# Kernel tuning notes

Measured on AMD Instinct MI355X. Metric: run time of the kernel, lower is better.

Reference implementation:

```python
import jax, jax.numpy as jnp
import numpy as np

EPS = 1e-5

def layer_norm(x, alpha, beta):
    mean = jnp.mean(x, axis=-1, keepdims=True)
    var = jnp.mean(jnp.square(x - mean), axis=-1, keepdims=True)
    return alpha * ((x - mean) / jnp.sqrt(var + EPS)) + beta

def setup_inputs() -> dict:
    key = jax.random.key(0)
    B, S, D, H = 4, 2048, 1024, 16
    Dff = 4 * D
    ks = jax.random.split(key, 8)
    inp = {
        "x": jax.random.normal(ks[0], (B, S, D), jnp.float32),
        "attention_mask": jnp.ones((B, S), jnp.int32),
        "ln1_alpha": jnp.ones((D,), jnp.float32),
        "ln1_beta": jnp.zeros((D,), jnp.float32),
        "ln2_alpha": jnp.ones((D,), jnp.float32),
        "ln2_beta": jnp.zeros((D,), jnp.float32),
        "Wq": jax.random.normal(ks[1], (D, D), jnp.float32) * 0.05,
        "Wk": jax.random.normal(ks[2], (D, D), jnp.float32) * 0.05,
        "Wv": jax.random.normal(ks[3], (D, D), jnp.float32) * 0.05,
        "Wo": jax.random.normal(ks[4], (D, D), jnp.float32) * 0.05,
        "W1": jax.random.normal(ks[5], (D, Dff), jnp.float32) * 0.02,
        "b1": jnp.zeros((Dff,), jnp.float32),
        "W2": jax.random.normal(ks[6], (Dff, D), jnp.float32) * 0.02,
        "b2": jnp.zeros((D,), jnp.float32),
    }
    return inp

def reference(x, attention_mask, ln1_alpha, ln1_beta, ln2_alpha, ln2_beta,
              Wq, Wk, Wv, Wo, W1, b1, W2, b2):
    B, S, D = x.shape
    H = 16
    dh = D // H

    # LN1 + self-attention
    y = layer_norm(x, ln1_alpha, ln1_beta)
    Q = (y @ Wq).reshape(B, S, H, dh).transpose(0, 2, 1, 3)  # [B,H,S,dh]
    K = (y @ Wk).reshape(B, S, H, dh).transpose(0, 2, 1, 3)
    V = (y @ Wv).reshape(B, S, H, dh).transpose(0, 2, 1, 3)

    scores = jnp.einsum("bhqd,bhkd->bhqk", Q, K) / jnp.sqrt(jnp.float32(dh))
    causal = jnp.tril(jnp.ones((S, S), jnp.float32))  # [S,S]
    tmask = attention_mask.astype(jnp.float32)  # [B,S]
    amask = causal[None, None, :, :] * tmask[:, None, None, :] * tmask[:, None, :, None]
    scores = jnp.where(amask > 0, scores, jnp.float32(-1e30))
    attn = jax.nn.softmax(scores, axis=-1)
    # dropout omitted (deterministic inference)
    ctx = jnp.einsum("bhqk,bhkd->bhqd", attn, V)
    ctx = ctx.transpose(0, 2, 1, 3).reshape(B, S, D)
    x = x + ctx @ Wo

    # LN2 + GELU FFN
    y = layer_norm(x, ln2_alpha, ln2_beta)
    h = jax.nn.gelu(y @ W1 + b1, approximate=False)
    x = x + (h @ W2 + b2)
    return x
```

## Files before the change

### kernel.cpp

```cpp
#include <hip/hip_runtime.h>
#include <math.h>

typedef unsigned short u16;
typedef unsigned int u32;
typedef __attribute__((ext_vector_type(4))) unsigned short u16x4;
typedef __attribute__((ext_vector_type(8))) short bf16x8;
typedef __attribute__((ext_vector_type(4))) float f32x4;

#define B_ 4
#define S_ 2048
#define D_ 1024
#define H_ 16
#define NT (B_*S_)
#define DFF 4096

static __device__ __forceinline__ float bf2f(u16 u) {
    return __uint_as_float(((u32)u) << 16);
}
static __device__ __forceinline__ u16 f2bf(float f) {
    u32 u = __float_as_uint(f);
    u32 r = (u + 0x7fffu + ((u >> 16) & 1u)) >> 16;
    return (u16)r;
}
static __device__ __forceinline__ void gload_lds16(const void* g, void* l) {
    __builtin_amdgcn_global_load_lds(
        (const __attribute__((address_space(1))) void*)g,
        (__attribute__((address_space(3))) void*)l, 16, 0, 0);
}

__global__ void transpose_f2b4(const float* __restrict__ s0, const float* __restrict__ s1,
                               const float* __restrict__ s2, const float* __restrict__ s3,
                               u16* __restrict__ d0, u16* __restrict__ d1,
                               u16* __restrict__ d2, u16* __restrict__ d3,
                               int R, int C) {
    const float* in = s0; u16* out = d0;
    if (blockIdx.z == 1) { in = s1; out = d1; }
    else if (blockIdx.z == 2) { in = s2; out = d2; }
    else if (blockIdx.z == 3) { in = s3; out = d3; }
    __shared__ float t[32][33];
    int c0 = blockIdx.x * 32, r0 = blockIdx.y * 32;
    int x = threadIdx.x, y = threadIdx.y;
    #pragma unroll
    for (int i = 0; i < 4; i++)
        t[y + i*8][x] = in[(long)(r0 + y + i*8) * C + c0 + x];
    __syncthreads();
    #pragma unroll
    for (int i = 0; i < 4; i++)
        out[(long)(c0 + y + i*8) * R + r0 + x] = f2bf(t[x][y + i*8]);
}

__global__ void transpose_f2b(const float* __restrict__ in, u16* __restrict__ out,
                              int R, int C) {
    __shared__ float t[32][33];
    int c0 = blockIdx.x * 32, r0 = blockIdx.y * 32;
    int x = threadIdx.x, y = threadIdx.y;
    #pragma unroll
    for (int i = 0; i < 4; i++)
        t[y + i*8][x] = in[(long)(r0 + y + i*8) * C + c0 + x];
    __syncthreads();
    #pragma unroll
    for (int i = 0; i < 4; i++)
        out[(long)(c0 + y + i*8) * R + r0 + x] = f2bf(t[x][y + i*8]);
}

__global__ void transpose_v(const u16* __restrict__ V, u16* __restrict__ Vt) {
    __shared__ u16 t[32][33];
    int z = blockIdx.z; int b = z >> 4, h = z & 15;
    int s0 = blockIdx.x * 32, d0 = blockIdx.y * 32;
    int x = threadIdx.x, y = threadIdx.y;
    const u16* in = V + ((long)b * S_ + s0) * D_ + h * 64 + d0;
    #pragma unroll
    for (int i = 0; i < 4; i++)
        t[y + i*8][x] = in[(long)(y + i*8) * D_ + x];
    __syncthreads();
    u16* out = Vt + ((long)z * 64 + d0) * S_ + s0;
    #pragma unroll
    for (int i = 0; i < 4; i++)
        out[(long)(y + i*8) * S_ + x] = t[x][y + i*8];
}

__global__ __launch_bounds__(256) void ln_kernel(
    const float* __restrict__ X, const float* __restrict__ alpha,
    const float* __restrict__ beta, u16* __restrict__ Y) {
    int row = blockIdx.x, tid = threadIdx.x;
    float4 xv = ((const float4*)(X + (long)row * D_))[tid];
    float v[4] = {xv.x, xv.y, xv.z, xv.w};
    float s = 0.f, ss = 0.f;
    #pragma unroll
    for (int i = 0; i < 4; i++) { s += v[i]; ss += v[i]*v[i]; }
    #pragma unroll
    for (int off = 32; off >= 1; off >>= 1) {
        s += __shfl_xor(s, off);
        ss += __shfl_xor(ss, off);
    }
    __shared__ float red[8];
    __shared__ float stats[2];
    int w = tid >> 6;
    if ((tid & 63) == 0) { red[w] = s; red[4 + w] = ss; }
    __syncthreads();
    if (tid == 0) {
        float S = red[0] + red[1] + red[2] + red[3];
        float SS = red[4] + red[5] + red[6] + red[7];
        float mean = S * (1.f / D_);
        float var = SS * (1.f / D_) - mean * mean;
        stats[0] = mean; stats[1] = rsqrtf(var + 1e-5f);
    }
    __syncthreads();
    float mean = stats[0], rstd = stats[1];
    float4 av = ((const float4*)alpha)[tid];
    float4 bv = ((const float4*)beta)[tid];
    u16x4 o;
    o[0] = f2bf((v[0] - mean) * rstd * av.x + bv.x);
    o[1] = f2bf((v[1] - mean) * rstd * av.y + bv.y);
    o[2] = f2bf((v[2] - mean) * rstd * av.z + bv.z);
    o[3] = f2bf((v[3] - mean) * rstd * av.w + bv.w);
    *(u16x4*)(Y + (long)row * D_ + tid * 4) = o;
}

#define BM 128
#define BN 128
#define BK 64

__global__ __launch_bounds__(256, 3) void gemm_bt(
    const u16* __restrict__ A,
    const u16* __restrict__ Bt0, const u16* __restrict__ Bt1, const u16* __restrict__ Bt2,
    void* __restrict__ C0, void* __restrict__ C1, void* __restrict__ C2,
    int M, int N, int K, int mode,
    const float* __restrict__ bias, const float* __restrict__ resid) {
    const u16* Bt = Bt0; void* C = C0;
    if (blockIdx.z == 1) { Bt = Bt1; C = C1; }
    else if (blockIdx.z == 2) { Bt = Bt2; C = C2; }

    __shared__ __align__(16) u16 Asm[BM * BK];
    __shared__ __align__(16) u16 Bsm[BN * BK];

    int tid = threadIdx.x;
    int lane = tid & 63, wave = tid >> 6;
    int l15 = lane & 15, quad = lane >> 4;
    int wm = wave & 1, wn = wave >> 1;
    long tm0 = (long)blockIdx.y * BM, tn0 = (long)blockIdx.x * BN;

    int srow = lane >> 3;
    int scol = (lane & 7) * 8;

    f32x4 acc[4][4] = {};

    for (int k0 = 0; k0 < K; k0 += BK) {
        __syncthreads();
        #pragma unroll
        for (int c = 0; c < 4; c++) {
            int chunk = wave * 4 + c;
            int row = chunk * 8 + srow;
            gload_lds16(&A[(tm0 + row) * (long)K + k0 + scol], &Asm[chunk * 512]);
            gload_lds16(&Bt[(tn0 + row) * (long)K + k0 + scol], &Bsm[chunk * 512]);
        }
        __syncthreads();
        #pragma unroll
        for (int ks = 0; ks < 2; ks++) {
            bf16x8 af[4], bfm[4];
            #pragma unroll
            for (int mt = 0; mt < 4; mt++)
                af[mt] = *(const bf16x8*)&Asm[(wm*64 + mt*16 + l15) * BK + ks*32 + quad*8];
            #pragma unroll
            for (int nt = 0; nt < 4; nt++)
                bfm[nt] = *(const bf16x8*)&Bsm[(wn*64 + nt*16 + l15) * BK + ks*32 + quad*8];
            #pragma unroll
            for (int mt = 0; mt < 4; mt++)
                #pragma unroll
                for (int nt = 0; nt < 4; nt++)
                    acc[mt][nt] = __builtin_amdgcn_mfma_f32_16x16x32_bf16(
                        af[mt], bfm[nt], acc[mt][nt], 0, 0, 0);
        }
    }

    #pragma unroll
    for (int mt = 0; mt < 4; mt++) {
        #pragma unroll
        for (int nt = 0; nt < 4; nt++) {
            #pragma unroll
            for (int i = 0; i < 4; i++) {
                long r = tm0 + wm*64 + mt*16 + quad*4 + i;
                long cn = tn0 + wn*64 + nt*16 + l15;
                long idx = r * N + cn;
                float val = acc[mt][nt][i];
                if (mode == 0) {
                    ((u16*)C)[idx] = f2bf(val);
                } else if (mode == 1) {
                    ((float*)C)[idx] = val + resid[idx];
                } else if (mode == 2) {
                    val += bias[cn];
                    val = 0.5f * val * (1.0f + erff(val * 0.70710678118654752f));
                    ((u16*)C)[idx] = f2bf(val);
                } else {
                    ((float*)C)[idx] = val + bias[cn] + resid[idx];
                }
            }
        }
    }
}

#define LDP 72

__global__ __launch_bounds__(256, 2) void attn_kernel(
    const u16* __restrict__ Q, const u16* __restrict__ Kg, const u16* __restrict__ Vt,
    const int* __restrict__ mask, u16* __restrict__ O) {
    __shared__ __align__(16) u16 Psm[4][32 * LDP];
    int tid = threadIdx.x;
    int lane = tid & 63, wave = tid >> 6;
    int l15 = lane & 15, quad = lane >> 4;
    int bh = blockIdx.x; int b = bh >> 4, h = bh & 15;
    int j = wave * 8 + blockIdx.y;
    long tokBase = (long)b * S_;
    const float SCL = 0.125f * 1.4426950408889634f;
    const float MMAX = 20.0f;

    const bf16x8 ones = {16256,16256,16256,16256,16256,16256,16256,16256};
    u16* Pw = Psm[wave];
    const int* mb = mask + b * S_;

    #pragma unroll
    for (int half = 0; half < 2; half++) {
        int t = half ? (63 - j) : j;
        int q0 = t * 32;

        bf16x8 aq[2][2];
        #pragma unroll
        for (int mt = 0; mt < 2; mt++) {
            const u16* qptr = Q + (tokBase + q0 + mt*16 + l15) * D_ + h * 64;
            aq[mt][0] = *(const bf16x8*)(qptr + quad * 8);
            aq[mt][1] = *(const bf16x8*)(qptr + 32 + quad * 8);
        }

        f32x4 o[2][4] = {};
        f32x4 lacc[2] = {};
        int ktiles = t / 2 + 1;

        for (int kt = 0; kt < ktiles; kt++) {
            int k0 = kt * 64;
            bf16x8 kb[4][2], vb[4][2];
            #pragma unroll
            for (int nt = 0; nt < 4; nt++) {
                const u16* kp = Kg + (tokBase + k0 + nt*16 + l15) * D_ + h * 64;
                kb[nt][0] = *(const bf16x8*)(kp + quad * 8);
                kb[nt][1] = *(const bf16x8*)(kp + 32 + quad * 8);
            }
            #pragma unroll
            for (int d = 0; d < 4; d++) {
                const u16* vp = Vt + ((long)bh * 64 + d*16 + l15) * S_ + k0;
                vb[d][0] = *(const bf16x8*)(vp + quad * 8);
                vb[d][1] = *(const bf16x8*)(vp + 32 + quad * 8);
            }

            f32x4 s[2][4] = {};
            #pragma unroll
            for (int nt = 0; nt < 4; nt++) {
                s[0][nt] = __builtin_amdgcn_mfma_f32_16x16x32_bf16(aq[0][0], kb[nt][0], s[0][nt], 0,0,0);
                s[0][nt] = __builtin_amdgcn_mfma_f32_16x16x32_bf16(aq[0][1], kb[nt][1], s[0][nt], 0,0,0);
                s[1][nt] = __builtin_amdgcn_mfma_f32_16x16x32_bf16(aq[1][0], kb[nt][0], s[1][nt], 0,0,0);
                s[1][nt] = __builtin_amdgcn_mfma_f32_16x16x32_bf16(aq[1][1], kb[nt][1], s[1][nt], 0,0,0);
            }

            int mk = 0;
            #pragma unroll
            for (int nt = 0; nt < 4; nt++)
                if (mb[k0 + nt*16 + l15] != 0) mk |= (1 << nt);

            #pragma unroll
            for (int mt = 0; mt < 2; mt++) {
                #pragma unroll
                for (int i = 0; i < 4; i++) {
                    int qq = q0 + mt*16 + quad*4 + i;
                    #pragma unroll
                    for (int nt = 0; nt < 4; nt++) {
                        int kc = k0 + nt*16 + l15;
                        float p = exp2f(fmaf(s[mt][nt][i], SCL, -MMAX));
                        p = (kc <= qq && ((mk >> nt) & 1)) ? p : 0.f;
                        Pw[(mt*16 + quad*4 + i) * LDP + nt*16 + l15] = f2bf(p);
                    }
                }
            }
            asm volatile("s_waitcnt lgkmcnt(0)" ::: "memory");

            #pragma unroll
            for (int hv = 0; hv < 2; hv++) {
                bf16x8 ap0 = *(const bf16x8*)&Pw[l15 * LDP + hv*32 + quad*8];
                bf16x8 ap1 = *(const bf16x8*)&Pw[(16 + l15) * LDP + hv*32 + quad*8];
                #pragma unroll
                for (int d = 0; d < 4; d++) {
                    o[0][d] = __builtin_amdgcn_mfma_f32_16x16x32_bf16(ap0, vb[d][hv], o[0][d], 0,0,0);
                    o[1][d] = __builtin_amdgcn_mfma_f32_16x16x32_bf16(ap1, vb[d][hv], o[1][d], 0,0,0);
                }
                lacc[0] = __builtin_amdgcn_mfma_f32_16x16x32_bf16(ap0, ones, lacc[0], 0,0,0);
                lacc[1] = __builtin_amdgcn_mfma_f32_16x16x32_bf16(ap1, ones, lacc[1], 0,0,0);
            }
        }

        #pragma unroll
        for (int mt = 0; mt < 2; mt++) {
            #pragma unroll
            for (int i = 0; i < 4; i++) {
                float inv = 1.f / lacc[mt][i];
                long r = tokBase + q0 + mt*16 + quad*4 + i;
                #pragma unroll
                for (int d = 0; d < 4; d++)
                    O[r * D_ + h*64 + d*16 + l15] = f2bf(o[mt][d][i] * inv);
            }
        }
    }
}

extern "C" void kernel_launch(void* const* d_in, const int* in_sizes, int n_in,
                              void* d_out, int out_size, void* d_ws, size_t ws_size,
                              hipStream_t stream) {
    const float* x    = (const float*)d_in[0];
    const int*   am   = (const int*)d_in[1];
    const float* ln1a = (const float*)d_in[2];
    const float* ln1b = (const float*)d_in[3];
    const float* ln2a = (const float*)d_in[4];
    const float* ln2b = (const float*)d_in[5];
    const float* wq   = (const float*)d_in[6];
    const float* wk   = (const float*)d_in[7];
    const float* wv   = (const float*)d_in[8];
    const float* wo   = (const float*)d_in[9];
    const float* w1   = (const float*)d_in[10];
    const float* b1   = (const float*)d_in[11];
    const float* w2   = (const float*)d_in[12];
    const float* b2   = (const float*)d_in[13];
    float* out = (float*)d_out;

    char* ws = (char*)d_ws;
    const size_t MB16 = (size_t)16 * 1024 * 1024;
    u16* y1      = (u16*)(ws + 0 * MB16);
    u16* q       = (u16*)(ws + 1 * MB16);
    u16* k       = (u16*)(ws + 2 * MB16);
    u16* v       = (u16*)(ws + 3 * MB16);
    u16* wqt     = (u16*)(ws + 4 * MB16 + 0 * (size_t)D_ * D_ * 2);
    u16* wkt     = (u16*)(ws + 4 * MB16 + 1 * (size_t)D_ * D_ * 2);
    u16* wvt     = (u16*)(ws + 4 * MB16 + 2 * (size_t)D_ * D_ * 2);
    u16* wot     = (u16*)(ws + 4 * MB16 + 3 * (size_t)D_ * D_ * 2);
    u16* y2      = y1;
    u16* w1t     = q;
    u16* w2t     = q + (size_t)D_ * DFF;
    u16* h_full  = k;
    u16* ctx     = v;
    u16*   vt  = (u16*)d_out;
    float* x1f = out;

    dim3 tb(32, 8);
    transpose_f2b4<<<dim3(D_/32, D_/32, 4), tb, 0, stream>>>(
        wq, wk, wv, wo, wqt, wkt, wvt, wot, D_, D_);

    ln_kernel<<<NT, 256, 0, stream>>>(x, ln1a, ln1b, y1);

    gemm_bt<<<dim3(D_/BN, NT/BM, 3), 256, 0, stream>>>(
        y1, wqt, wkt, wvt, q, k, v, NT, D_, D_, 0, nullptr, nullptr);

    transpose_v<<<dim3(S_/32, 2, B_*H_), tb, 0, stream>>>(v, vt);

    attn_kernel<<<dim3(B_*H_, 8), 256, 0, stream>>>(q, k, vt, am, ctx);

    gemm_bt<<<dim3(D_/BN, NT/BM, 1), 256, 0, stream>>>(
        ctx, wot, wot, wot, x1f, x1f, x1f, NT, D_, D_, 1, nullptr, x);

    transpose_f2b<<<dim3(DFF/32, D_/32), tb, 0, stream>>>(w1, w1t, D_, DFF);
    transpose_f2b<<<dim3(D_/32, DFF/32), tb, 0, stream>>>(w2, w2t, DFF, D_);

    ln_kernel<<<NT, 256, 0, stream>>>(x1f, ln2a, ln2b, y2);

    gemm_bt<<<dim3(DFF/BN, NT/BM, 1), 256, 0, stream>>>(
        y2, w1t, w1t, w1t, h_full, h_full, h_full, NT, DFF, D_, 2, b1, nullptr);
    gemm_bt<<<dim3(D_/BN, NT/BM, 1), 256, 0, stream>>>(
        h_full, w2t, w2t, w2t, out, out, out, NT, D_, DFF, 3, b2, x1f);
}
```

Baseline: 696.4 us.

## Double-buffer GEMM LDS tiles, swizzle workgroups, split attention key loop across wave pairs

The GEMM now double-buffers its LDS tiles, issuing the next tile's global-to-LDS loads before computing on the current one, which removes one barrier per k-step. It also remaps workgroup IDs with an XCD-aware swizzle to improve L2 locality. The attention kernel splits each query tile's key loop between two waves and merges their partial outputs and row sums through LDS. This doubles the attention grid and raises the occupancy hint, at the cost of extra LDS, two block barriers, and halved GEMM occupancy.

```diff
diff --git a/kernel.cpp b/kernel.cpp
--- a/kernel.cpp
+++ b/kernel.cpp
@@ -121,7 +121,28 @@
 #define BN 128
 #define BK 64
 
-__global__ __launch_bounds__(256, 3) void gemm_bt(
+static __device__ __forceinline__ void mfma_tile(
+    const u16* As, const u16* Bs, f32x4 (&acc)[4][4],
+    int wm, int wn, int l15, int quad) {
+    #pragma unroll
+    for (int ks = 0; ks < 2; ks++) {
+        bf16x8 af[4], bfm[4];
+        #pragma unroll
+        for (int mt = 0; mt < 4; mt++)
+            af[mt] = *(const bf16x8*)&As[(wm*64 + mt*16 + l15) * BK + ks*32 + quad*8];
+        #pragma unroll
+        for (int nt = 0; nt < 4; nt++)
+            bfm[nt] = *(const bf16x8*)&Bs[(wn*64 + nt*16 + l15) * BK + ks*32 + quad*8];
+        #pragma unroll
+        for (int mt = 0; mt < 4; mt++)
+            #pragma unroll
+            for (int nt = 0; nt < 4; nt++)
+                acc[mt][nt] = __builtin_amdgcn_mfma_f32_16x16x32_bf16(
+                    af[mt], bfm[nt], acc[mt][nt], 0, 0, 0);
+    }
+}
+
+__global__ __launch_bounds__(256, 2) void gemm_bt(
     const u16* __restrict__ A,
     const u16* __restrict__ Bt0, const u16* __restrict__ Bt1, const u16* __restrict__ Bt2,
     void* __restrict__ C0, void* __restrict__ C1, void* __restrict__ C2,
@@ -131,47 +152,56 @@
     if (blockIdx.z == 1) { Bt = Bt1; C = C1; }
     else if (blockIdx.z == 2) { Bt = Bt2; C = C2; }
 
-    __shared__ __align__(16) u16 Asm[BM * BK];
-    __shared__ __align__(16) u16 Bsm[BN * BK];
+    __shared__ __align__(16) u16 Asm[2][BM * BK];
+    __shared__ __align__(16) u16 Bsm[2][BN * BK];
 
     int tid = threadIdx.x;
     int lane = tid & 63, wave = tid >> 6;
     int l15 = lane & 15, quad = lane >> 4;
     int wm = wave & 1, wn = wave >> 1;
-    long tm0 = (long)blockIdx.y * BM, tn0 = (long)blockIdx.x * BN;
+
+    int nx = gridDim.x;
+    int nwg = nx * gridDim.y;
+    int orig = blockIdx.y * nx + blockIdx.x;
+    int wgid = (orig & 7) * (nwg >> 3) + (orig >> 3);
+    int bx = wgid % nx, by = wgid / nx;
+    long tm0 = (long)by * BM, tn0 = (long)bx * BN;
 
     int srow = lane >> 3;
     int scol = (lane & 7) * 8;
 
+    const u16* aB[4]; const u16* bB[4];
+    #pragma unroll
+    for (int c = 0; c < 4; c++) {
+        int row = (wave * 4 + c) * 8 + srow;
+        aB[c] = A  + (tm0 + row) * (long)K + scol;
+        bB[c] = Bt + (tn0 + row) * (long)K + scol;
+    }
+
     f32x4 acc[4][4] = {};
 
-    for (int k0 = 0; k0 < K; k0 += BK) {
-        __syncthreads();
+    #pragma unroll
+    for (int c = 0; c < 4; c++) {
+        int chunk = wave * 4 + c;
+        gload_lds16(aB[c], &Asm[0][chunk * 512]);
+        gload_lds16(bB[c], &Bsm[0][chunk * 512]);
+    }
+    __syncthreads();
+
+    int steps = K / BK;
+    for (int k = 0; k < steps - 1; k++) {
+        int nb = (k + 1) & 1;
+        long koff = (long)(k + 1) * BK;
         #pragma unroll
         for (int c = 0; c < 4; c++) {
             int chunk = wave * 4 + c;
-            int row = chunk * 8 + srow;
-            gload_lds16(&A[(tm0 + row) * (long)K + k0 + scol], &Asm[chunk * 512]);
-            gload_lds16(&Bt[(tn0 + row) * (long)K + k0 + scol], &Bsm[chunk * 512]);
-        }
+            gload_lds16(aB[c] + koff, &Asm[nb][chunk * 512]);
+            gload_lds16(bB[c] + koff, &Bsm[nb][chunk * 512]);
+        }
+        mfma_tile(&Asm[k & 1][0], &Bsm[k & 1][0], acc, wm, wn, l15, quad);
         __syncthreads();
-        #pragma unroll
-        for (int ks = 0; ks < 2; ks++) {
-            bf16x8 af[4], bfm[4];
-            #pragma unroll
-            for (int mt = 0; mt < 4; mt++)
-                af[mt] = *(const bf16x8*)&Asm[(wm*64 + mt*16 + l15) * BK + ks*32 + quad*8];
-            #pragma unroll
-            for (int nt = 0; nt < 4; nt++)
-                bfm[nt] = *(const bf16x8*)&Bsm[(wn*64 + nt*16 + l15) * BK + ks*32 + quad*8];
-            #pragma unroll
-            for (int mt = 0; mt < 4; mt++)
-                #pragma unroll
-                for (int nt = 0; nt < 4; nt++)
-                    acc[mt][nt] = __builtin_amdgcn_mfma_f32_16x16x32_bf16(
-                        af[mt], bfm[nt], acc[mt][nt], 0, 0, 0);
-        }
-    }
+    }
+    mfma_tile(&Asm[(steps - 1) & 1][0], &Bsm[(steps - 1) & 1][0], acc, wm, wn, l15, quad);
 
     #pragma unroll
     for (int mt = 0; mt < 4; mt++) {
@@ -201,15 +231,18 @@
 
 #define LDP 72
 
-__global__ __launch_bounds__(256, 2) void attn_kernel(
+__global__ __launch_bounds__(256, 4) void attn_kernel(
     const u16* __restrict__ Q, const u16* __restrict__ Kg, const u16* __restrict__ Vt,
     const int* __restrict__ mask, u16* __restrict__ O) {
     __shared__ __align__(16) u16 Psm[4][32 * LDP];
+    __shared__ __align__(16) float Mrg[2][64][40];
     int tid = threadIdx.x;
     int lane = tid & 63, wave = tid >> 6;
     int l15 = lane & 15, quad = lane >> 4;
     int bh = blockIdx.x; int b = bh >> 4, h = bh & 15;
-    int j = wave * 8 + blockIdx.y;
+    int pslot = wave >> 1;
+    int hk = wave & 1;
+    int j = blockIdx.y * 2 + pslot;
     long tokBase = (long)b * S_;
     const float SCL = 0.125f * 1.4426950408889634f;
     const float MMAX = 20.0f;
@@ -235,7 +268,7 @@
         f32x4 lacc[2] = {};
         int ktiles = t / 2 + 1;
 
-        for (int kt = 0; kt < ktiles; kt++) {
+        for (int kt = hk; kt < ktiles; kt += 2) {
             int k0 = kt * 64;
             bf16x8 kb[4][2], vb[4][2];
             #pragma unroll
@@ -295,17 +328,40 @@
             }
         }
 
-        #pragma unroll
-        for (int mt = 0; mt < 2; mt++) {
-            #pragma unroll
-            for (int i = 0; i < 4; i++) {
-                float inv = 1.f / lacc[mt][i];
-                long r = tokBase + q0 + mt*16 + quad*4 + i;
+        if (hk == 1) {
+            float* m = &Mrg[pslot][lane][0];
+            #pragma unroll
+            for (int mt = 0; mt < 2; mt++)
                 #pragma unroll
                 for (int d = 0; d < 4; d++)
-                    O[r * D_ + h*64 + d*16 + l15] = f2bf(o[mt][d][i] * inv);
-            }
-        }
+                    *(f32x4*)&m[(mt*4 + d)*4] = o[mt][d];
+            *(f32x4*)&m[32] = lacc[0];
+            *(f32x4*)&m[36] = lacc[1];
+        }
+        __syncthreads();
+        if (hk == 0) {
+            const float* m = &Mrg[pslot][lane][0];
+            #pragma unroll
+            for (int mt = 0; mt < 2; mt++)
+                #pragma unroll
+                for (int d = 0; d < 4; d++)
+                    o[mt][d] += *(const f32x4*)&m[(mt*4 + d)*4];
+            lacc[0] += *(const f32x4*)&m[32];
+            lacc[1] += *(const f32x4*)&m[36];
+
+            #pragma unroll
+            for (int mt = 0; mt < 2; mt++) {
+                #pragma unroll
+                for (int i = 0; i < 4; i++) {
+                    float inv = 1.f / lacc[mt][i];
+                    long r = tokBase + q0 + mt*16 + quad*4 + i;
+                    #pragma unroll
+                    for (int d = 0; d < 4; d++)
+                        O[r * D_ + h*64 + d*16 + l15] = f2bf(o[mt][d][i] * inv);
+                }
+            }
+        }
+        __syncthreads();
     }
 }
 
@@ -357,7 +413,7 @@
 
     transpose_v<<<dim3(S_/32, 2, B_*H_), tb, 0, stream>>>(v, vt);
 
-    attn_kernel<<<dim3(B_*H_, 8), 256, 0, stream>>>(q, k, vt, am, ctx);
+    attn_kernel<<<dim3(B_*H_, 16), 256, 0, stream>>>(q, k, vt, am, ctx);
 
     gemm_bt<<<dim3(D_/BN, NT/BM, 1), 256, 0, stream>>>(
         ctx, wot, wot, wot, x1f, x1f, x1f, NT, D_, D_, 1, nullptr, x);
```

Result: slower. 806.2 us (+15.8%).
